# Optimization experiments

Hardware: AMD Instinct MI355X
Metric: run time of the kernel (lower is better)

## Reference

```python
import jax, jax.numpy as jnp
import numpy as np

N = 16384
INPUT_DIM = 256
HIDDEN1 = 128
HIDDEN2 = 64


def setup_inputs() -> dict:
    key = jax.random.key(0)
    ks = jax.random.split(key, 8)
    X = jax.random.normal(ks[0], (N, INPUT_DIM), dtype=jnp.float32)
    adj = jax.random.uniform(ks[1], (N, N), dtype=jnp.float32)
    # Xavier-uniform style scaling for weights
    def xavier(k, shape):
        fan_in, fan_out = shape
        lim = float(np.sqrt(6.0 / (fan_in + fan_out)))
        return jax.random.uniform(k, shape, dtype=jnp.float32, minval=-lim, maxval=lim)
    W1 = xavier(ks[2], (INPUT_DIM, HIDDEN1))
    Wm = xavier(ks[3], (HIDDEN1, HIDDEN2))
    Ws = xavier(ks[4], (HIDDEN1, HIDDEN2))
    Wp = xavier(ks[5], (HIDDEN2, HIDDEN2))
    bp = jnp.zeros((HIDDEN2,), dtype=jnp.float32)
    noise = jax.random.normal(ks[6], (N, HIDDEN2), dtype=jnp.float32)
    return {"X": X, "adj": adj, "W1": W1, "Wm": Wm, "Ws": Ws,
            "Wp": Wp, "bp": bp, "noise": noise}


def _gcn(x, adj, W, activation):
    # GraphConvSparse: adj @ (x @ W) then activation
    h = adj @ (x @ W)
    return activation(h)


def reference(X, adj, W1, Wm, Ws, Wp, bp, noise):
    # base GCN with ReLU
    hidden = _gcn(X, adj, W1, jax.nn.relu)            # [N, hidden1]
    # mean branch: identity-activation GCN then Linear projection
    Z = _gcn(hidden, adj, Wm, lambda x: x)            # [N, hidden2]
    mean = Z @ Wp + bp                                # [N, hidden2]
    # logstd branch with clamp(max=10)
    logstd = _gcn(hidden, adj, Ws, lambda x: x)
    logstd = jnp.minimum(logstd, 10.0)
    # reparameterization trick
    sampled_z = noise * jnp.exp(logstd) + mean        # [N, hidden2]
    return sampled_z
```

## Files before the change

### kernel.cpp

```cpp
#include <hip/hip_runtime.h>


typedef __bf16 bf16_t;
typedef __attribute__((ext_vector_type(4))) __bf16 bf16x4;
typedef __attribute__((ext_vector_type(8))) __bf16 bf16x8;
typedef __attribute__((ext_vector_type(16))) float f32x16;
typedef __attribute__((ext_vector_type(4)))  float f32x4;

#define N_NODES 16384
#define MFMA3(ACC, A, B) \
    ACC = __builtin_amdgcn_mfma_f32_32x32x16_bf16(A, B, ACC, 0, 0, 0)

__device__ __forceinline__ int frag_off(int r, int c) {
    int K16  = r >> 4;
    int cblk = c >> 5;
    int g    = (r >> 3) & 1;
    int lane = (c & 31) + (g << 5);
    return ((K16 * 4 + cblk) << 9) + (lane << 3) + (r & 7);
}

__device__ __forceinline__ float4 relu_add4(float4 a, float4 b) {
    float4 r;
    r.x = fmaxf(a.x + b.x, 0.f); r.y = fmaxf(a.y + b.y, 0.f);
    r.z = fmaxf(a.z + b.z, 0.f); r.w = fmaxf(a.w + b.w, 0.f);
    return r;
}

template<int K, bool FUSED, bool ADD2>
__global__ __launch_bounds__(256)
void producer_kernel(const float* __restrict__ A,
                     const float* __restrict__ A2,
                     const float* __restrict__ W,
                     const float* __restrict__ Wa,
                     const float* __restrict__ Wb,
                     bf16_t* __restrict__ Bh,
                     bf16_t* __restrict__ Bl)
{
    __shared__ float As[32][128];
    __shared__ float Wsh[32][128];
    const int t    = threadIdx.x;
    const int row0 = blockIdx.x * 128;
    const int tc   = t & 15, tr = t >> 4;

    float acc[8][8];
    #pragma unroll
    for (int i = 0; i < 8; ++i)
        #pragma unroll
        for (int j = 0; j < 8; ++j) acc[i][j] = 0.f;

    const int ra = t >> 1, ks = (t & 1) << 4;
    const int wk = t >> 3, wc = (t & 7) << 4;

    for (int k0 = 0; k0 < K; k0 += 32) {
        const float* ap = A + (size_t)(row0 + ra) * K + k0 + ks;
        float4 a0 = *(const float4*)(ap);
        float4 a1 = *(const float4*)(ap + 4);
        float4 a2 = *(const float4*)(ap + 8);
        float4 a3 = *(const float4*)(ap + 12);
        if (ADD2) {
            const float* ap2 = A2 + (size_t)(row0 + ra) * K + k0 + ks;
            a0 = relu_add4(a0, *(const float4*)(ap2));
            a1 = relu_add4(a1, *(const float4*)(ap2 + 4));
            a2 = relu_add4(a2, *(const float4*)(ap2 + 8));
            a3 = relu_add4(a3, *(const float4*)(ap2 + 12));
        }
        float4 w0, w1, w2, w3;
        if (!FUSED) {
            const float* wp = W + (size_t)(k0 + wk) * 128 + wc;
            w0 = *(const float4*)(wp);     w1 = *(const float4*)(wp + 4);
            w2 = *(const float4*)(wp + 8); w3 = *(const float4*)(wp + 12);
        } else {
            const float* wp = (wc < 64) ? (Wa + (size_t)(k0 + wk) * 64 + wc)
                                        : (Wb + (size_t)(k0 + wk) * 64 + (wc - 64));
            w0 = *(const float4*)(wp);     w1 = *(const float4*)(wp + 4);
            w2 = *(const float4*)(wp + 8); w3 = *(const float4*)(wp + 12);
        }
        __syncthreads();
        {
            float tmp[16] = {a0.x,a0.y,a0.z,a0.w, a1.x,a1.y,a1.z,a1.w,
                             a2.x,a2.y,a2.z,a2.w, a3.x,a3.y,a3.z,a3.w};
            #pragma unroll
            for (int j = 0; j < 16; ++j) As[ks + j][ra] = tmp[j];
            *(float4*)&Wsh[wk][wc     ] = w0;
            *(float4*)&Wsh[wk][wc +  4] = w1;
            *(float4*)&Wsh[wk][wc +  8] = w2;
            *(float4*)&Wsh[wk][wc + 12] = w3;
        }
        __syncthreads();
        #pragma unroll 4
        for (int k = 0; k < 32; ++k) {
            float av[8], wv[8];
            *(float4*)&av[0] = *(const float4*)&As[k][8 * tr];
            *(float4*)&av[4] = *(const float4*)&As[k][8 * tr + 4];
            *(float4*)&wv[0] = *(const float4*)&Wsh[k][8 * tc];
            *(float4*)&wv[4] = *(const float4*)&Wsh[k][8 * tc + 4];
            #pragma unroll
            for (int i = 0; i < 8; ++i)
                #pragma unroll
                for (int j = 0; j < 8; ++j)
                    acc[i][j] = fmaf(av[i], wv[j], acc[i][j]);
        }
    }

    #pragma unroll
    for (int i = 0; i < 8; ++i) {
        int r = row0 + 8 * tr + i;
        #pragma unroll
        for (int j = 0; j < 8; ++j) {
            int c = 8 * tc + j;
            float v = acc[i][j];
            bf16_t h = (bf16_t)v;
            bf16_t l = (bf16_t)(v - (float)h);
            int off = frag_off(r, c);
            Bh[off] = h;
            Bl[off] = l;
        }
    }
}

struct BSet { bf16x8 h[4]; bf16x8 l[4]; };

__global__ __launch_bounds__(512, 2)
void adj_gemm_kernel(const float* __restrict__ adj,
                     const bf16_t* __restrict__ Bh,
                     const bf16_t* __restrict__ Bl,
                     float* __restrict__ P0,
                     float* __restrict__ P1)
{
    __shared__ __align__(16) bf16_t AsH[128 * 256];
    __shared__ __align__(16) bf16_t AsL[128 * 256];
    const int t    = threadIdx.x;
    const int lane = t & 63;
    const int w    = t >> 6;
    const int mt   = blockIdx.x >> 1;
    const int kh   = blockIdx.x & 1;
    const int row0 = mt << 7;
    const int hi32 = lane >> 5;
    float* const outP = kh ? P1 : P0;

    const float* aBase = adj + (size_t)(row0 + (w << 4)) * 16384
                             + (kh << 13) + (lane << 2);

    int wIdx[16];
    #pragma unroll
    for (int j = 0; j < 16; ++j) {
        int row = (w << 4) + j;
        wIdx[j] = (row << 8) + ((((lane >> 2) ^ (row & 15)) << 4)
                                + ((lane & 3) << 2));
    }

    const int rh   = w >> 2, cq = w & 3;
    const int frow = (rh << 6) + (lane & 31);
    const int rbase0 = (frow << 8) + (hi32 << 3);
    const int rbase1 = ((frow + 32) << 8) + (hi32 << 3);
    const int rx     = frow & 15;

    const int tb   = (cq << 9) + (lane << 3);
    const int sub0 = kh << 7;

    f32x16 acc0, acc1;
    #pragma unroll
    for (int i = 0; i < 16; ++i) { acc0[i] = 0.f; acc1[i] = 0.f; }

    f32x4 ar[16];
    BSet S0, S1;

    auto loadAdj = [&](int mac) {
        const float* p = aBase + (mac << 8);
        #pragma unroll
        for (int j = 0; j < 16; ++j)
            ar[j] = __builtin_nontemporal_load((const f32x4*)(p + (size_t)j * 16384));
    };
    auto cvtWrite = [&]() {
        #pragma unroll
        for (int j = 0; j < 16; ++j) {
            bf16x4 hv, lv;
            #pragma unroll
            for (int e = 0; e < 4; ++e) {
                float v = ar[j][e];
                bf16_t h = (bf16_t)v;
                hv[e] = h;
                lv[e] = (bf16_t)(v - (float)h);
            }
            *(bf16x4*)&AsH[wIdx[j]] = hv;
            *(bf16x4*)&AsL[wIdx[j]] = lv;
        }
    };
    auto loadB = [&](BSet& S, int sub) {
        const size_t base = ((size_t)sub << 13) + tb;
        #pragma unroll
        for (int s = 0; s < 4; ++s) {
            S.h[s] = *(const bf16x8*)(Bh + base + (s << 11));
            S.l[s] = *(const bf16x8*)(Bl + base + (s << 11));
        }
    };
    auto computeS = [&](const BSet& S, int s) {
        #pragma unroll
        for (int k16 = 0; k16 < 4; ++k16) {
            const int u  = (s << 2) + k16;
            const int o  = (u ^ rx) << 4;
            bf16x8 ah0 = *(const bf16x8*)&AsH[rbase0 + o];
            bf16x8 al0 = *(const bf16x8*)&AsL[rbase0 + o];
            bf16x8 ah1 = *(const bf16x8*)&AsH[rbase1 + o];
            bf16x8 al1 = *(const bf16x8*)&AsL[rbase1 + o];
            MFMA3(acc0, ah0, S.h[k16]);
            MFMA3(acc1, ah1, S.h[k16]);
            MFMA3(acc0, ah0, S.l[k16]);
            MFMA3(acc1, ah1, S.l[k16]);
            MFMA3(acc0, al0, S.h[k16]);
            MFMA3(acc1, al1, S.h[k16]);
        }
    };

#define SYNC_LDS() do { asm volatile("s_waitcnt lgkmcnt(0)" ::: "memory"); \
                        __builtin_amdgcn_s_barrier(); } while (0)

    loadAdj(0);
    for (int m = 0; m < 32; ++m) {
        cvtWrite();
        SYNC_LDS();
        const int sb = sub0 + (m << 2);
        loadB(S0, sb + 0);
        if (m < 31) loadAdj(m + 1);
        computeS(S0, 0);
        loadB(S1, sb + 1);  computeS(S1, 1);
        loadB(S0, sb + 2);  computeS(S0, 2);
        loadB(S1, sb + 3);  computeS(S1, 3);
        SYNC_LDS();
    }
#undef SYNC_LDS

    const int col = (cq << 5) + (lane & 31);
    const int rw  = row0 + (rh << 6) + (hi32 << 2);
    #pragma unroll
    for (int q = 0; q < 16; ++q) {
        int r = rw + (q & 3) + ((q >> 2) << 3);
        outP[(size_t)r * 128 + col]        = acc0[q];
        outP[(size_t)(r + 32) * 128 + col] = acc1[q];
    }
}

__global__ __launch_bounds__(256)
void final_kernel(const float* __restrict__ T0,
                  const float* __restrict__ T1,
                  const float* __restrict__ Wp,
                  const float* __restrict__ bp,
                  const float* __restrict__ noise,
                  float* __restrict__ out)
{
    __shared__ float Wps[64][64];
    __shared__ float Ts[64][64];
    const int t = threadIdx.x;
    const int row0 = blockIdx.x * 64;
    {
        int k = t >> 2, c0 = (t & 3) << 4;
        #pragma unroll
        for (int i = 0; i < 4; ++i)
            *(float4*)&Wps[k][c0 + 4 * i] = *(const float4*)&Wp[(size_t)k * 64 + c0 + 4 * i];
        #pragma unroll
        for (int i = 0; i < 4; ++i) {
            float4 z0 = *(const float4*)&T0[(size_t)(row0 + k) * 128 + c0 + 4 * i];
            float4 z1 = *(const float4*)&T1[(size_t)(row0 + k) * 128 + c0 + 4 * i];
            float4 zs; zs.x = z0.x + z1.x; zs.y = z0.y + z1.y;
            zs.z = z0.z + z1.z; zs.w = z0.w + z1.w;
            *(float4*)&Ts[k][c0 + 4 * i] = zs;
        }
    }
    __syncthreads();

    const int r  = t >> 2;
    const int c0 = (t & 3) << 4;
    float acc[16];
    #pragma unroll
    for (int j = 0; j < 16; ++j) acc[j] = bp[c0 + j];
    for (int k = 0; k < 64; ++k) {
        float a = Ts[r][k];
        #pragma unroll
        for (int j = 0; j < 16; ++j) acc[j] = fmaf(a, Wps[k][c0 + j], acc[j]);
    }
    const int grow = row0 + r;
    #pragma unroll
    for (int j = 0; j < 16; ++j) {
        size_t li = (size_t)grow * 128 + 64 + c0 + j;
        float ls = T0[li] + T1[li];
        ls = fminf(ls, 10.0f);
        out[(size_t)grow * 64 + c0 + j] =
            noise[(size_t)grow * 64 + c0 + j] * __expf(ls) + acc[j];
    }
}

extern "C" void kernel_launch(void* const* d_in, const int* in_sizes, int n_in,
                              void* d_out, int out_size, void* d_ws, size_t ws_size,
                              hipStream_t stream) {
    const float* X     = (const float*)d_in[0];
    const float* adj   = (const float*)d_in[1];
    const float* W1    = (const float*)d_in[2];
    const float* Wm    = (const float*)d_in[3];
    const float* Wsv   = (const float*)d_in[4];
    const float* Wp    = (const float*)d_in[5];
    const float* bp    = (const float*)d_in[6];
    const float* noise = (const float*)d_in[7];
    float* out = (float*)d_out;

    char* ws = (char*)d_ws;
    bf16_t* Bh = (bf16_t*)ws;
    bf16_t* Bl = (bf16_t*)(ws + (4u << 20));
    float*  P0 = (float*)(ws + (8u << 20));
    float*  P1 = (float*)(ws + (16u << 20));

    producer_kernel<256, false, false><<<128, 256, 0, stream>>>(
        X, nullptr, W1, nullptr, nullptr, Bh, Bl);
    adj_gemm_kernel<<<256, 512, 0, stream>>>(adj, Bh, Bl, P0, P1);
    producer_kernel<128, true, true><<<128, 256, 0, stream>>>(
        P0, P1, nullptr, Wm, Wsv, Bh, Bl);
    adj_gemm_kernel<<<256, 512, 0, stream>>>(adj, Bh, Bl, P0, P1);
    final_kernel<<<256, 256, 0, stream>>>(P0, P1, Wp, bp, noise, out);
}
```

Baseline: 726.7 us.

## Cache bf16 hi/lo split of adj during first GEMM and reuse it in second

The first adjacency GEMM now also writes its bf16 high/low split of adj to a workspace buffer in a pre-swizzled tile layout. A new second GEMM kernel streams that 1 GB bf16 copy instead of re-reading the 1 GB fp32 adj and re-converting it. It also drops the K-split, so the final kernel reads a single partial sum. Total traffic stays similar: an extra 1 GB write in the first pass and an equal-size read in the second. The change mainly removes the conversion work and the partial-sum reduction, and risks slowing the first GEMM with the extra stores.

```diff
diff --git a/kernel.cpp b/kernel.cpp
--- a/kernel.cpp
+++ b/kernel.cpp
@@ -120,12 +120,13 @@
 
 struct BSet { bf16x8 h[4]; bf16x8 l[4]; };
 
-__global__ __launch_bounds__(512, 2)
-void adj_gemm_kernel(const float* __restrict__ adj,
-                     const bf16_t* __restrict__ Bh,
-                     const bf16_t* __restrict__ Bl,
-                     float* __restrict__ P0,
-                     float* __restrict__ P1)
+__global__ __launch_bounds__(512)
+void adj_gemm_store_kernel(const float* __restrict__ adj,
+                           const bf16_t* __restrict__ Bh,
+                           const bf16_t* __restrict__ Bl,
+                           float* __restrict__ P0,
+                           float* __restrict__ P1,
+                           bf16_t* __restrict__ adjT)
 {
     __shared__ __align__(16) bf16_t AsH[128 * 256];
     __shared__ __align__(16) bf16_t AsL[128 * 256];
@@ -141,13 +142,19 @@
     const float* aBase = adj + (size_t)(row0 + (w << 4)) * 16384
                              + (kh << 13) + (lane << 2);
 
-    int wIdx[16];
+    int wIdx[16], stOff[16];
     #pragma unroll
     for (int j = 0; j < 16; ++j) {
         int row = (w << 4) + j;
         wIdx[j] = (row << 8) + ((((lane >> 2) ^ (row & 15)) << 4)
                                 + ((lane & 3) << 2));
-    }
+        int rl = row & 63;
+        stOff[j] = (rl << 9) + ((((lane >> 2) ^ (rl & 15)) << 5)
+                                + ((lane & 3) << 3));
+    }
+    const int mt2 = 2 * mt + (w >> 2 >= 1 ? (w >= 4 ? 1 : 0) : 0);
+    char* const stBase = (char*)adjT
+                       + (((size_t)(2 * mt + (w >= 4)) * 64 + kh * 32) << 16);
 
     const int rh   = w >> 2, cq = w & 3;
     const int frow = (rh << 6) + (lane & 31);
@@ -171,7 +178,8 @@
         for (int j = 0; j < 16; ++j)
             ar[j] = __builtin_nontemporal_load((const f32x4*)(p + (size_t)j * 16384));
     };
-    auto cvtWrite = [&]() {
+    auto cvtWrite = [&](int mac) {
+        char* const sp = stBase + ((size_t)mac << 16);
         #pragma unroll
         for (int j = 0; j < 16; ++j) {
             bf16x4 hv, lv;
@@ -184,6 +192,8 @@
             }
             *(bf16x4*)&AsH[wIdx[j]] = hv;
             *(bf16x4*)&AsL[wIdx[j]] = lv;
+            __builtin_nontemporal_store(hv, (bf16x4*)(sp + stOff[j]));
+            __builtin_nontemporal_store(lv, (bf16x4*)(sp + stOff[j] + 32768));
         }
     };
     auto loadB = [&](BSet& S, int sub) {
@@ -217,7 +227,7 @@
 
     loadAdj(0);
     for (int m = 0; m < 32; ++m) {
-        cvtWrite();
+        cvtWrite(m);
         SYNC_LDS();
         const int sb = sub0 + (m << 2);
         loadB(S0, sb + 0);
@@ -240,9 +250,97 @@
     }
 }
 
+__global__ __launch_bounds__(512)
+void adj_gemm2_kernel(const bf16_t* __restrict__ adjT,
+                      const bf16_t* __restrict__ Bh,
+                      const bf16_t* __restrict__ Bl,
+                      float* __restrict__ T)
+{
+    __shared__ __align__(16) bf16_t As[32768];
+    const int t    = threadIdx.x;
+    const int lane = t & 63;
+    const int w    = t >> 6;
+    const int mt2  = blockIdx.x;
+    const int row0 = mt2 << 6;
+    const int hi32 = lane >> 5;
+
+    const char* const src0 = (const char*)adjT + ((size_t)mt2 << 22);
+
+    const int rh   = w >> 2, cq = w & 3;
+    const int frow = (rh << 5) + (lane & 31);
+    const int rbase = (frow << 8) + (hi32 << 3);
+    const int rx    = frow & 15;
+
+    const int tb = (cq << 9) + (lane << 3);
+
+    f32x16 acc;
+    #pragma unroll
+    for (int i = 0; i < 16; ++i) acc[i] = 0.f;
+
+    bf16x8 st[8];
+    BSet S0, S1;
+
+    auto loadSt = [&](int mac) {
+        const char* p = src0 + ((size_t)mac << 16) + (t << 4);
+        #pragma unroll
+        for (int r = 0; r < 8; ++r)
+            st[r] = __builtin_nontemporal_load((const bf16x8*)(p + r * 8192));
+    };
+    auto dsWriteSt = [&]() {
+        #pragma unroll
+        for (int r = 0; r < 8; ++r)
+            *(bf16x8*)((char*)As + (t << 4) + r * 8192) = st[r];
+    };
+    auto loadB = [&](BSet& S, int sub) {
+        const size_t base = ((size_t)sub << 13) + tb;
+        #pragma unroll
+        for (int s = 0; s < 4; ++s) {
+            S.h[s] = *(const bf16x8*)(Bh + base + (s << 11));
+            S.l[s] = *(const bf16x8*)(Bl + base + (s << 11));
+        }
+    };
+    auto computeS = [&](const BSet& S, int s) {
+        #pragma unroll
+        for (int k16 = 0; k16 < 4; ++k16) {
+            const int u  = (s << 2) + k16;
+            const int o  = (u ^ rx) << 4;
+            bf16x8 ah = *(const bf16x8*)&As[rbase + o];
+            bf16x8 al = *(const bf16x8*)&As[rbase + o + 16384];
+            MFMA3(acc, ah, S.h[k16]);
+            MFMA3(acc, ah, S.l[k16]);
+            MFMA3(acc, al, S.h[k16]);
+        }
+    };
+
+#define SYNC_LDS() do { asm volatile("s_waitcnt lgkmcnt(0)" ::: "memory"); \
+                        __builtin_amdgcn_s_barrier(); } while (0)
+
+    loadSt(0);
+    for (int m = 0; m < 64; ++m) {
+        dsWriteSt();
+        SYNC_LDS();
+        const int sb = m << 2;
+        loadB(S0, sb + 0);
+        if (m < 63) loadSt(m + 1);
+        computeS(S0, 0);
+        loadB(S1, sb + 1);  computeS(S1, 1);
+        loadB(S0, sb + 2);  computeS(S0, 2);
+        loadB(S1, sb + 3);  computeS(S1, 3);
+        SYNC_LDS();
+    }
+#undef SYNC_LDS
+
+    const int col = (cq << 5) + (lane & 31);
+    const int rw  = row0 + (rh << 5) + (hi32 << 2);
+    #pragma unroll
+    for (int q = 0; q < 16; ++q) {
+        int r = rw + (q & 3) + ((q >> 2) << 3);
+        T[(size_t)r * 128 + col] = acc[q];
+    }
+}
+
 __global__ __launch_bounds__(256)
-void final_kernel(const float* __restrict__ T0,
-                  const float* __restrict__ T1,
+void final_kernel(const float* __restrict__ T,
                   const float* __restrict__ Wp,
                   const float* __restrict__ bp,
                   const float* __restrict__ noise,
@@ -258,13 +356,9 @@
         for (int i = 0; i < 4; ++i)
             *(float4*)&Wps[k][c0 + 4 * i] = *(const float4*)&Wp[(size_t)k * 64 + c0 + 4 * i];
         #pragma unroll
-        for (int i = 0; i < 4; ++i) {
-            float4 z0 = *(const float4*)&T0[(size_t)(row0 + k) * 128 + c0 + 4 * i];
-            float4 z1 = *(const float4*)&T1[(size_t)(row0 + k) * 128 + c0 + 4 * i];
-            float4 zs; zs.x = z0.x + z1.x; zs.y = z0.y + z1.y;
-            zs.z = z0.z + z1.z; zs.w = z0.w + z1.w;
-            *(float4*)&Ts[k][c0 + 4 * i] = zs;
-        }
+        for (int i = 0; i < 4; ++i)
+            *(float4*)&Ts[k][c0 + 4 * i] =
+                *(const float4*)&T[(size_t)(row0 + k) * 128 + c0 + 4 * i];
     }
     __syncthreads();
 
@@ -281,8 +375,7 @@
     const int grow = row0 + r;
     #pragma unroll
     for (int j = 0; j < 16; ++j) {
-        size_t li = (size_t)grow * 128 + 64 + c0 + j;
-        float ls = T0[li] + T1[li];
+        float ls = T[(size_t)grow * 128 + 64 + c0 + j];
         ls = fminf(ls, 10.0f);
         out[(size_t)grow * 64 + c0 + j] =
             noise[(size_t)grow * 64 + c0 + j] * __expf(ls) + acc[j];
@@ -303,16 +396,17 @@
     float* out = (float*)d_out;
 
     char* ws = (char*)d_ws;
-    bf16_t* Bh = (bf16_t*)ws;
-    bf16_t* Bl = (bf16_t*)(ws + (4u << 20));
-    float*  P0 = (float*)(ws + (8u << 20));
-    float*  P1 = (float*)(ws + (16u << 20));
+    bf16_t* Bh   = (bf16_t*)ws;
+    bf16_t* Bl   = (bf16_t*)(ws + (4u << 20));
+    float*  P0   = (float*)(ws + (8u << 20));
+    float*  P1   = (float*)(ws + (16u << 20));
+    bf16_t* adjT = (bf16_t*)(ws + (24u << 20));
 
     producer_kernel<256, false, false><<<128, 256, 0, stream>>>(
         X, nullptr, W1, nullptr, nullptr, Bh, Bl);
-    adj_gemm_kernel<<<256, 512, 0, stream>>>(adj, Bh, Bl, P0, P1);
+    adj_gemm_store_kernel<<<256, 512, 0, stream>>>(adj, Bh, Bl, P0, P1, adjT);
     producer_kernel<128, true, true><<<128, 256, 0, stream>>>(
         P0, P1, nullptr, Wm, Wsv, Bh, Bl);
-    adj_gemm_kernel<<<256, 512, 0, stream>>>(adj, Bh, Bl, P0, P1);
-    final_kernel<<<256, 256, 0, stream>>>(P0, P1, Wp, bp, noise, out);
-}
+    adj_gemm2_kernel<<<256, 512, 0, stream>>>(adjT, Bh, Bl, P0);
+    final_kernel<<<256, 256, 0, stream>>>(P0, Wp, bp, noise, out);
+}
```

After: 889.2 us. 1.22x slower.
